# Kernel tuning notes

Measured on AMD Instinct MI355X. Metric: run time of the kernel, lower is better.

## Reference

```python
import jax, jax.numpy as jnp
import numpy as np

B, S, V, D = 65536, 51, 64, 64  # batch, seq_len (= max_length), vocab (= output_dimension), output dim
E, H1, H2 = 4, 5, 7             # embedding dim and hidden widths of the tiny MLP


def setup_inputs() -> dict:
    key = jax.random.key(0)
    ks = jax.random.split(key, 8)
    x = jax.random.randint(ks[0], (B, S), 0, V, dtype=jnp.int64)
    # Per-position parameters, stacked along the leading S axis (one tiny net per position).
    emb = jax.random.normal(ks[1], (S, V, E), dtype=jnp.float32)
    W1 = jax.random.normal(ks[2], (S, H1, E), dtype=jnp.float32) * 0.5
    b1 = jnp.zeros((S, H1), dtype=jnp.float32)
    W2 = jax.random.normal(ks[3], (S, H2, H1), dtype=jnp.float32) * 0.5
    b2 = jnp.zeros((S, H2), dtype=jnp.float32)
    W3 = jax.random.normal(ks[4], (S, D, H2), dtype=jnp.float32) * 0.5
    b3 = jnp.zeros((S, D), dtype=jnp.float32)
    return {"x": x, "emb": emb, "W1": W1, "b1": b1, "W2": W2, "b2": b2, "W3": W3, "b3": b3}


def reference(x, emb, W1, b1, W2, b2, W3, b3):
    S_ = emb.shape[0]
    pos = jnp.arange(S_)[None, :]                       # [1, S]
    e = emb[pos, x]                                     # [B, S, E] per-position embedding lookup
    h1 = jax.nn.leaky_relu(jnp.einsum('bse,she->bsh', e, W1) + b1)   # [B, S, H1]
    h2 = jax.nn.leaky_relu(jnp.einsum('bsh,sgh->bsg', h1, W2) + b2)  # [B, S, H2]
    y = jnp.tanh(jnp.einsum('bsg,sdg->bsd', h2, W3) + b3)            # [B, S, D]
    return jnp.sum(y, axis=1)                           # [B, D] sum over positions
```

## Files before the change

kernel.cpp:

```cpp
#include <hip/hip_runtime.h>

constexpr int S  = 51;
constexpr int V  = 64;
constexpr int E  = 4;
constexpr int H1 = 5;
constexpr int H2 = 7;
constexpr int D  = 64;

__global__ void build_table_kernel(const float* __restrict__ emb,
                                   const float* __restrict__ W1,
                                   const float* __restrict__ b1,
                                   const float* __restrict__ W2,
                                   const float* __restrict__ b2,
                                   const float* __restrict__ W3,
                                   const float* __restrict__ b3,
                                   float* __restrict__ Y) {
  const int sv = blockIdx.x;
  const int s  = sv >> 6;
  const int d  = threadIdx.x;

  float e[E];
#pragma unroll
  for (int i = 0; i < E; ++i) e[i] = emb[sv * E + i];

  float h1[H1];
#pragma unroll
  for (int h = 0; h < H1; ++h) {
    float a = b1[s * H1 + h];
#pragma unroll
    for (int i = 0; i < E; ++i) a = fmaf(W1[(s * H1 + h) * E + i], e[i], a);
    h1[h] = (a >= 0.f) ? a : 0.01f * a;
  }

  float h2[H2];
#pragma unroll
  for (int g = 0; g < H2; ++g) {
    float a = b2[s * H2 + g];
#pragma unroll
    for (int h = 0; h < H1; ++h) a = fmaf(W2[(s * H2 + g) * H1 + h], h1[h], a);
    h2[g] = (a >= 0.f) ? a : 0.01f * a;
  }

  float a = b3[s * D + d];
#pragma unroll
  for (int g = 0; g < H2; ++g) a = fmaf(W3[(s * D + d) * H2 + g], h2[g], a);

  Y[sv * D + d] = tanhf(a);
}

__global__ __launch_bounds__(256) void gather_sum_kernel(
    const int* __restrict__ x, const float* __restrict__ Y,
    float* __restrict__ out, int B) {
  const int lane  = threadIdx.x & 63;
  const int wid   = threadIdx.x >> 6;
  const int bbase = (blockIdx.x * 4 + wid) * 4;
  if (bbase >= B) return;

  int tok0 = 0, tok1 = 0, tok2 = 0, tok3 = 0;
  if (lane < S) {
    tok0 = x[(bbase + 0) * S + lane];
    tok1 = x[(bbase + 1) * S + lane];
    tok2 = x[(bbase + 2) * S + lane];
    tok3 = x[(bbase + 3) * S + lane];
  }

  float acc0 = 0.f, acc1 = 0.f, acc2 = 0.f, acc3 = 0.f;
#pragma unroll 4
  for (int s = 0; s < S; ++s) {
    const float* Ys = Y + (s << 12);
    const int t0 = __shfl(tok0, s);
    const int t1 = __shfl(tok1, s);
    const int t2 = __shfl(tok2, s);
    const int t3 = __shfl(tok3, s);
    acc0 += Ys[(t0 << 6) + lane];
    acc1 += Ys[(t1 << 6) + lane];
    acc2 += Ys[(t2 << 6) + lane];
    acc3 += Ys[(t3 << 6) + lane];
  }

  out[(bbase + 0) * D + lane] = acc0;
  out[(bbase + 1) * D + lane] = acc1;
  out[(bbase + 2) * D + lane] = acc2;
  out[(bbase + 3) * D + lane] = acc3;
}

extern "C" void kernel_launch(void* const* d_in, const int* in_sizes, int n_in,
                              void* d_out, int out_size, void* d_ws, size_t ws_size,
                              hipStream_t stream) {
  const int*   x   = (const int*)d_in[0];
  const float* emb = (const float*)d_in[1];
  const float* W1  = (const float*)d_in[2];
  const float* b1  = (const float*)d_in[3];
  const float* W2  = (const float*)d_in[4];
  const float* b2  = (const float*)d_in[5];
  const float* W3  = (const float*)d_in[6];
  const float* b3  = (const float*)d_in[7];

  const int B = in_sizes[0] / S;
  float* Y = (float*)d_ws;

  build_table_kernel<<<S * V, D, 0, stream>>>(emb, W1, b1, W2, b2, W3, b3, Y);

  const int blocks = (B + 15) / 16;
  gather_sum_kernel<<<blocks, 256, 0, stream>>>(x, Y, (float*)d_out, B);
}
```

Measured before the change: 118.3 us.

## Store lookup table in fp16 and gather 16-byte vectors per lane

```diff
diff --git a/kernel.cpp b/kernel.cpp
--- a/kernel.cpp
+++ b/kernel.cpp
@@ -1,4 +1,5 @@
 #include <hip/hip_runtime.h>
+#include <hip/hip_fp16.h>
 
 constexpr int S  = 51;
 constexpr int V  = 64;
@@ -14,7 +15,7 @@
                                    const float* __restrict__ b2,
                                    const float* __restrict__ W3,
                                    const float* __restrict__ b3,
-                                   float* __restrict__ Y) {
+                                   __half* __restrict__ Y) {
   const int sv = blockIdx.x;
   const int s  = sv >> 6;
   const int d  = threadIdx.x;
@@ -45,43 +46,48 @@
 #pragma unroll
   for (int g = 0; g < H2; ++g) a = fmaf(W3[(s * D + d) * H2 + g], h2[g], a);
 
-  Y[sv * D + d] = tanhf(a);
+  Y[sv * D + d] = __float2half(tanhf(a));
 }
 
 __global__ __launch_bounds__(256) void gather_sum_kernel(
-    const int* __restrict__ x, const float* __restrict__ Y,
+    const int* __restrict__ x, const __half* __restrict__ Y,
     float* __restrict__ out, int B) {
   const int lane  = threadIdx.x & 63;
   const int wid   = threadIdx.x >> 6;
-  const int bbase = (blockIdx.x * 4 + wid) * 4;
-  if (bbase >= B) return;
+  const int li    = lane & 7;
+  const int bbase = (blockIdx.x * 4 + wid) * 8;
+  const int row   = bbase + (lane >> 3);
 
-  int tok0 = 0, tok1 = 0, tok2 = 0, tok3 = 0;
-  if (lane < S) {
-    tok0 = x[(bbase + 0) * S + lane];
-    tok1 = x[(bbase + 1) * S + lane];
-    tok2 = x[(bbase + 2) * S + lane];
-    tok3 = x[(bbase + 3) * S + lane];
+  int tok[7];
+#pragma unroll
+  for (int j = 0; j < 7; ++j) {
+    const int s = j * 8 + li;
+    tok[j] = (s < S) ? x[row * S + s] : 0;
   }
 
-  float acc0 = 0.f, acc1 = 0.f, acc2 = 0.f, acc3 = 0.f;
-#pragma unroll 4
+  float acc[8];
+#pragma unroll
+  for (int k = 0; k < 8; ++k) acc[k] = 0.f;
+
+  const __half* Ybase = Y + (li << 3);
+  const int rgsel = lane & 56;
+
+#pragma unroll
   for (int s = 0; s < S; ++s) {
-    const float* Ys = Y + (s << 12);
-    const int t0 = __shfl(tok0, s);
-    const int t1 = __shfl(tok1, s);
-    const int t2 = __shfl(tok2, s);
-    const int t3 = __shfl(tok3, s);
-    acc0 += Ys[(t0 << 6) + lane];
-    acc1 += Ys[(t1 << 6) + lane];
-    acc2 += Ys[(t2 << 6) + lane];
-    acc3 += Ys[(t3 << 6) + lane];
+    const int t = __shfl(tok[s >> 3], rgsel | (s & 7), 64);
+    const uint4 v = *reinterpret_cast<const uint4*>(Ybase + (s << 12) + (t << 6));
+    union { uint4 u; __half2 h[4]; } cv; cv.u = v;
+#pragma unroll
+    for (int k = 0; k < 4; ++k) {
+      const float2 f = __half22float2(cv.h[k]);
+      acc[2 * k]     += f.x;
+      acc[2 * k + 1] += f.y;
+    }
   }
 
-  out[(bbase + 0) * D + lane] = acc0;
-  out[(bbase + 1) * D + lane] = acc1;
-  out[(bbase + 2) * D + lane] = acc2;
-  out[(bbase + 3) * D + lane] = acc3;
+  float4* o = reinterpret_cast<float4*>(out + row * D + (li << 3));
+  o[0] = make_float4(acc[0], acc[1], acc[2], acc[3]);
+  o[1] = make_float4(acc[4], acc[5], acc[6], acc[7]);
 }
 
 extern "C" void kernel_launch(void* const* d_in, const int* in_sizes, int n_in,
@@ -97,10 +103,10 @@
   const float* b3  = (const float*)d_in[7];
 
   const int B = in_sizes[0] / S;
-  float* Y = (float*)d_ws;
+  __half* Y = (__half*)d_ws;
 
   build_table_kernel<<<S * V, D, 0, stream>>>(emb, W1, b1, W2, b2, W3, b3, Y);
 
-  const int blocks = (B + 15) / 16;
+  const int blocks = B / 32;
   gather_sum_kernel<<<blocks, 256, 0, stream>>>(x, Y, (float*)d_out, B);
 }
```

Result: faster. 97.26 us (-17.8%).
